# Kernel optimization log

Hardware: AMD Instinct MI355X
Metric: run time of the kernel (lower is better)

## Reference

```python
import jax, jax.numpy as jnp
import numpy as np

STATE_LEN = 128

def _layernorm(x, eps=1e-5):
    m = jnp.mean(x, axis=-1, keepdims=True)
    v = jnp.mean(jnp.square(x - m), axis=-1, keepdims=True)
    return (x - m) * jax.lax.rsqrt(v + eps)

def setup_inputs() -> dict:
    key = jax.random.key(0)
    ks = jax.random.split(key, 20)
    B, S, L = 2, 2048, STATE_LEN
    Din, Dk, Dv, H = 1024, 64, 64, 8
    T = S + 2 * L  # 2304
    x = jax.random.normal(ks[0], (B, T, Din), jnp.float32)
    def w(k, dout):
        return jax.random.normal(k, (H, Din, dout), jnp.float32) / np.sqrt(Din).astype(np.float32)
    inp = {
        'x': x,
        'ln_g':  1.0 + 0.02 * jax.random.normal(ks[1], (H, Din), jnp.float32),
        'ln_b':  0.02 * jax.random.normal(ks[2], (H, Din), jnp.float32),
        'ln_gs': 1.0 + 0.02 * jax.random.normal(ks[3], (H, Din), jnp.float32),
        'ln_bs': 0.02 * jax.random.normal(ks[4], (H, Din), jnp.float32),
        'ln_ge': 1.0 + 0.02 * jax.random.normal(ks[5], (H, Din), jnp.float32),
        'ln_be': 0.02 * jax.random.normal(ks[6], (H, Din), jnp.float32),
        'Wq':   w(ks[7], Dk),  'Wk':   w(ks[8], Dk),  'Wv':   w(ks[9], Dv),
        'Wq_s': w(ks[10], Dk), 'Wk_s': w(ks[11], Dk), 'Wv_s': w(ks[12], Dv),
        'Wq_e': w(ks[13], Dk), 'Wk_e': w(ks[14], Dk), 'Wv_e': w(ks[15], Dv),
        'offset': 0,
    }
    return inp

def _forward(x, ln_g, ln_b, ln_gs, ln_bs, ln_ge, ln_be,
             Wq, Wk, Wv, Wq_s, Wk_s, Wv_s, Wq_e, Wk_e, Wv_e):
    L = STATE_LEN
    B, T, Din = x.shape
    # extract_state: start state, middle sequence, end state
    xs, xm, xe = x[:, :L], x[:, L:T - L], x[:, T - L:]
    # LayerNorm stats are parameter-free; per-head affine applied after
    ns, nm, ne = _layernorm(xs), _layernorm(xm), _layernorm(xe)
    def aff(n, g, b):  # [B,seg,Din] -> [B,H,seg,Din]
        return n[:, None, :, :] * g[None, :, None, :] + b[None, :, None, :]
    hs, hm, he = aff(ns, ln_gs, ln_bs), aff(nm, ln_g, ln_b), aff(ne, ln_ge, ln_be)
    proj = lambda h, W: jnp.einsum('bhsd,hde->bhse', h, W)
    q = jnp.concatenate([proj(hs, Wq_s), proj(hm, Wq), proj(he, Wq_e)], axis=2)
    k = jnp.concatenate([proj(hs, Wk_s), proj(hm, Wk), proj(he, Wk_e)], axis=2)
    v = jnp.concatenate([proj(hs, Wv_s), proj(hm, Wv), proj(he, Wv_e)], axis=2)
    Dk = q.shape[-1]
    scores = jnp.einsum('bhsd,bhtd->bhst', q, k) / jnp.asarray(np.sqrt(Dk), q.dtype)
    # Faithful to the torch code: a FLOAT tril-of-ones mask is passed to SDPA,
    # which ADDS it to the scores (it does not set -inf anywhere).
    mask = jnp.tril(jnp.ones((T, T), scores.dtype))
    att = jax.nn.softmax(scores + mask, axis=-1)
    out = jnp.einsum('bhst,bhtd->bhsd', att, v)  # [B,H,T,Dv]
    H, Dv = out.shape[1], out.shape[3]
    # torch.concat over heads on last dim
    return out.transpose(0, 2, 1, 3).reshape(B, T, H * Dv)

def reference(x, ln_g, ln_b, ln_gs, ln_bs, ln_ge, ln_be,
              Wq, Wk, Wv, Wq_s, Wk_s, Wv_s, Wq_e, Wk_e, Wv_e, offset):
    # offset unused: position_embedders are None in this configuration
    return _forward(x, ln_g, ln_b, ln_gs, ln_bs, ln_ge, ln_be,
                    Wq, Wk, Wv, Wq_s, Wk_s, Wv_s, Wq_e, Wk_e, Wv_e)
```

## Files before the change

### kernel.cpp

```cpp
#include <hip/hip_runtime.h>

#define TSEQ 2304
#define DIN  1024
#define NH   8
#define DD   64
#define NC   1536
#define MROWS 4608
#define L2E  1.44269504f
#define EF   2.71828183f

typedef __attribute__((ext_vector_type(8))) short bf16x8;
typedef __attribute__((ext_vector_type(4))) float f32x4;
typedef __attribute__((ext_vector_type(4))) unsigned short u16x4;

__device__ __forceinline__ unsigned short f2bf(float f){
    union { float f; unsigned int u; } x; x.f = f;
    unsigned int r = x.u + 0x7FFFu + ((x.u >> 16) & 1u);
    return (unsigned short)(r >> 16);
}

__device__ __forceinline__ float exp2raw(float x){
    float r;
    asm("v_exp_f32 %0, %1" : "=v"(r) : "v"(x));
    return r;
}

__device__ __forceinline__ unsigned int cvtpk(float a, float b){
    unsigned int r;
    asm("v_cvt_pk_bf16_f32 %0, %1, %2" : "=v"(r) : "v"(a), "v"(b));
    return r;
}

__device__ __forceinline__ void gload_lds16(const void* g, void* l){
    __builtin_amdgcn_global_load_lds(
        (const __attribute__((address_space(1))) void*)g,
        (__attribute__((address_space(3))) void*)l, 16, 0, 0);
}

struct WArgs {
    const float* W[9];
    const float* g[3];
    const float* bv[3];
};

__global__ __launch_bounds__(256) void k_pre(WArgs a, const float* __restrict__ x,
                                             unsigned short* __restrict__ wb,
                                             float* __restrict__ bias,
                                             unsigned short* __restrict__ nrm)
{
    __shared__ float lds[64][65];
    __shared__ float red[4][64];
    __shared__ float r1[4], r2[4];
    const int bid = blockIdx.x;
    const int tid = threadIdx.x;
    if (bid < 1152){
        const int dt = bid & 15, h = (bid >> 4) & 7, sp = bid >> 7;
        const int seg = sp / 3, proj = sp % 3;
        const float* W = a.W[seg*3 + proj];
        const float* g = a.g[seg];
        const int d0 = dt * 64;
        {
            const int e = tid & 63, rq = tid >> 6;
#pragma unroll
            for (int rr = 0; rr < 16; ++rr){
                const int dl = rr*4 + rq;
                lds[dl][e] = W[((size_t)h*DIN + d0 + dl)*DD + e];
            }
        }
        __syncthreads();
        {
            const int dl = tid & 63, eq = tid >> 6;
            const int n0 = proj*512 + h*64;
            const float gv = g[h*DIN + d0 + dl];
#pragma unroll
            for (int rr = 0; rr < 16; ++rr){
                const int el = eq*16 + rr;
                wb[((size_t)seg*NC + n0 + el)*DIN + d0 + dl] = f2bf(lds[dl][el] * gv);
            }
        }
    } else if (bid < 1224){
        const int u = bid - 1152;
        const int h = u & 7, sp = u >> 3;
        const int seg = sp / 3, proj = sp % 3;
        const float* W  = a.W[seg*3 + proj];
        const float* bv = a.bv[seg];
        const int e = tid & 63, dc = tid >> 6;
        float sum = 0.f;
        for (int i = 0; i < 256; ++i){
            const int d = dc*256 + i;
            sum += bv[h*DIN + d] * W[((size_t)h*DIN + d)*DD + e];
        }
        red[dc][e] = sum;
        __syncthreads();
        if (dc == 0)
            bias[seg*NC + proj*512 + h*64 + e] = red[0][e] + red[1][e] + red[2][e] + red[3][e];
    } else {
        const int row = bid - 1224;
        const float* xr = x + (size_t)row * DIN;
        f32x4 v = *(const f32x4*)&xr[tid*4];
        float s1 = v[0]+v[1]+v[2]+v[3];
        float s2 = v[0]*v[0]+v[1]*v[1]+v[2]*v[2]+v[3]*v[3];
#pragma unroll
        for (int m = 1; m < 64; m <<= 1){ s1 += __shfl_xor(s1, m); s2 += __shfl_xor(s2, m); }
        const int wid = tid >> 6;
        if ((tid & 63) == 0){ r1[wid] = s1; r2[wid] = s2; }
        __syncthreads();
        s1 = r1[0]+r1[1]+r1[2]+r1[3];
        s2 = r2[0]+r2[1]+r2[2]+r2[3];
        const float mean = s1 * (1.f/1024.f);
        const float var  = s2 * (1.f/1024.f) - mean*mean;
        const float rstd = rsqrtf(var + 1e-5f);
        u16x4 ov;
#pragma unroll
        for (int j = 0; j < 4; ++j) ov[j] = f2bf((v[j]-mean)*rstd);
        *(u16x4*)&nrm[(size_t)row*DIN + tid*4] = ov;
    }
}

__global__ __launch_bounds__(256) void k_gemm(
    const unsigned short* __restrict__ A,
    const unsigned short* __restrict__ Wb,
    const float* __restrict__ bias,
    unsigned short* __restrict__ qo,
    unsigned short* __restrict__ ko,
    unsigned short* __restrict__ vt)
{
    __shared__ unsigned short As[128*64];
    __shared__ unsigned short Bs[128*64];
    const int mt = blockIdx.x, nt = blockIdx.y;
    const int row0 = mt*128, n0 = nt*128;
    const int rloc = row0 % TSEQ;
    const int seg = (rloc < 128) ? 0 : (rloc < 2176 ? 1 : 2);
    const unsigned short* Bp = Wb + (size_t)seg * NC * DIN;
    const int tid = threadIdx.x;
    const int wid = tid >> 6, lane = tid & 63;
    const int wr = wid >> 1, wc = wid & 1;
    const int lr = lane & 15, lg = lane >> 4;
    const int rsub = lane >> 3;
    const int cgx  = (lane & 7) ^ rsub;
    f32x4 acc[4][4];
#pragma unroll
    for (int m = 0; m < 4; ++m)
#pragma unroll
        for (int n = 0; n < 4; ++n) acc[m][n] = (f32x4){0.f,0.f,0.f,0.f};

    for (int kt = 0; kt < DIN/64; ++kt){
        const int k0 = kt*64;
        __syncthreads();
#pragma unroll
        for (int i = 0; i < 4; ++i){
            const int c = wid*4 + i;
            const int r = c*8 + rsub;
            gload_lds16(&A [(size_t)(row0 + r)*DIN + k0 + cgx*8], &As[c*512]);
            gload_lds16(&Bp[(size_t)(n0  + r)*DIN + k0 + cgx*8], &Bs[c*512]);
        }
        __syncthreads();
#pragma unroll
        for (int ks = 0; ks < 2; ++ks){
            bf16x8 af[4], bfr[4];
#pragma unroll
            for (int m = 0; m < 4; ++m)
                af[m]  = *(const bf16x8*)&As[(wr*64 + m*16 + lr)*64 + (((ks*4 + lg) ^ (lr & 7))*8)];
#pragma unroll
            for (int n = 0; n < 4; ++n)
                bfr[n] = *(const bf16x8*)&Bs[(wc*64 + n*16 + lr)*64 + (((ks*4 + lg) ^ (lr & 7))*8)];
#pragma unroll
            for (int m = 0; m < 4; ++m)
#pragma unroll
                for (int n = 0; n < 4; ++n)
                    acc[m][n] = __builtin_amdgcn_mfma_f32_16x16x32_bf16(af[m], bfr[n], acc[m][n], 0, 0, 0);
        }
    }
    const int b_ = row0 / TSEQ;
    const int t0 = row0 - b_ * TSEQ;
#pragma unroll
    for (int m = 0; m < 4; ++m){
#pragma unroll
        for (int n = 0; n < 4; ++n){
            const int nglob = n0 + wc*64 + n*16 + lr;
            const float bs = bias[seg*NC + nglob];
            const int proj = nglob >> 9, hh = (nglob >> 6) & 7, e = nglob & 63;
            if (proj < 2){
                unsigned short* op = (proj == 0) ? qo : ko;
                const float scale = (proj == 0) ? 0.125f * L2E : 1.0f;
                const size_t ob = ((size_t)(b_*NH + hh) * TSEQ) * DD + e;
#pragma unroll
                for (int j = 0; j < 4; ++j){
                    const int t = t0 + wr*64 + m*16 + 4*lg + j;
                    op[ob + (size_t)t * DD] = f2bf((acc[m][n][j] + bs) * scale);
                }
            } else {
                unsigned short* vp = vt + ((size_t)(b_*NH + hh)*DD + e)*TSEQ;
                const int t = t0 + wr*64 + m*16 + 4*lg;
                u16x4 pk;
#pragma unroll
                for (int j = 0; j < 4; ++j) pk[j] = f2bf(acc[m][n][j] + bs);
                *(u16x4*)&vp[t] = pk;
            }
        }
    }
}

__global__ __launch_bounds__(256) void k_attn(
    const unsigned short* __restrict__ Q,
    const unsigned short* __restrict__ K,
    const unsigned short* __restrict__ Vt,
    float* __restrict__ po0,
    float* __restrict__ po1,
    float* __restrict__ out2,
    float* __restrict__ pl)
{
    __shared__ unsigned short Ks[2][64*64];
    __shared__ unsigned short Vs[2][64*64];
    __shared__ unsigned short Plds[4][32][72];
    const int qtb = blockIdx.x;
    const int bh  = blockIdx.y;
    const int z   = blockIdx.z;
    const int kt0 = z*12, kt1 = kt0 + 12;
    const int tid  = threadIdx.x;
    const int w    = tid >> 6;
    const int lane = tid & 63;
    const int lr = lane & 15, lg = lane >> 4;
    const size_t qkb = (size_t)bh * TSEQ * DD;
    const size_t vtb = (size_t)bh * DD * TSEQ;
    const int q0w = qtb*128 + w*32;
    const int kd  = qtb*2 + (w >> 1);

    const int rsub = lane >> 3;
    const int cgx  = (lane & 7) ^ rsub;
    const char* Kbase  = (const char*)(K  + qkb);
    const char* Vtbase = (const char*)(Vt + vtb);

    bf16x8 aq[2][2];
#pragma unroll
    for (int qg = 0; qg < 2; ++qg)
#pragma unroll
        for (int ks = 0; ks < 2; ++ks)
            aq[qg][ks] = *(const bf16x8*)&Q[qkb + (size_t)(q0w + qg*16 + lr)*DD + ks*32 + lg*8];

    float lsum[2] = {0.f, 0.f};
    f32x4 o[2][4];
#pragma unroll
    for (int qg = 0; qg < 2; ++qg)
#pragma unroll
        for (int nd = 0; nd < 4; ++nd) o[qg][nd] = (f32x4){0.f,0.f,0.f,0.f};

    auto stage = [&](int kt, int b){
        const int kn = kt*64;
#pragma unroll
        for (int i = 0; i < 2; ++i){
            const int c = w*2 + i;
            const int r = c*8 + rsub;
            gload_lds16(Kbase  + (size_t)(kn + r)*128 + cgx*16,              &Ks[b][c*512]);
            gload_lds16(Vtbase + (size_t)r*(TSEQ*2) + (size_t)kn*2 + cgx*16, &Vs[b][c*512]);
        }
    };

    stage(kt0, 0);
    __syncthreads();

    unsigned int* PldsW = (unsigned int*)&Plds[w][0][0];

    int buf = 0;
    for (int kt = kt0; kt < kt1; ++kt){
        const int kc0 = kt*64;
        if (kt + 1 < kt1) stage(kt + 1, buf ^ 1);
        bf16x8 bk[2][4];
#pragma unroll
        for (int ks = 0; ks < 2; ++ks)
#pragma unroll
            for (int ns = 0; ns < 4; ++ns)
                bk[ks][ns] = *(const bf16x8*)&Ks[buf][(ns*16 + lr)*64 + (((4*ks + lg) ^ (lr & 7))*8)];
        f32x4 s[2][4];
#pragma unroll
        for (int qg = 0; qg < 2; ++qg)
#pragma unroll
            for (int ns = 0; ns < 4; ++ns) s[qg][ns] = (f32x4){0.f,0.f,0.f,0.f};
#pragma unroll
        for (int qg = 0; qg < 2; ++qg)
#pragma unroll
            for (int ks = 0; ks < 2; ++ks)
#pragma unroll
                for (int ns = 0; ns < 4; ++ns)
                    s[qg][ns] = __builtin_amdgcn_mfma_f32_16x16x32_bf16(bk[ks][ns], aq[qg][ks], s[qg][ns], 0, 0, 0);
        if (kt == kd){
#pragma unroll
            for (int qg = 0; qg < 2; ++qg){
                lsum[qg] *= EF;
#pragma unroll
                for (int nd = 0; nd < 4; ++nd)
#pragma unroll
                    for (int j = 0; j < 4; ++j) o[qg][nd][j] *= EF;
                const int qr = q0w + qg*16 + lr;
#pragma unroll
                for (int ns = 0; ns < 4; ++ns){
                    const int kb = kc0 + ns*16 + 4*lg;
                    float p0 = exp2raw(s[qg][ns][0] + ((kb + 0 <= qr) ? L2E : 0.f));
                    float p1 = exp2raw(s[qg][ns][1] + ((kb + 1 <= qr) ? L2E : 0.f));
                    float p2 = exp2raw(s[qg][ns][2] + ((kb + 2 <= qr) ? L2E : 0.f));
                    float p3 = exp2raw(s[qg][ns][3] + ((kb + 3 <= qr) ? L2E : 0.f));
                    lsum[qg] += (p0 + p1) + (p2 + p3);
                    PldsW[(qg*16 + lr)*36 + ns*8 + 2*lg + 0] = cvtpk(p0, p1);
                    PldsW[(qg*16 + lr)*36 + ns*8 + 2*lg + 1] = cvtpk(p2, p3);
                }
            }
        } else {
#pragma unroll
            for (int qg = 0; qg < 2; ++qg){
#pragma unroll
                for (int ns = 0; ns < 4; ++ns){
                    float p0 = exp2raw(s[qg][ns][0]);
                    float p1 = exp2raw(s[qg][ns][1]);
                    float p2 = exp2raw(s[qg][ns][2]);
                    float p3 = exp2raw(s[qg][ns][3]);
                    lsum[qg] += (p0 + p1) + (p2 + p3);
                    PldsW[(qg*16 + lr)*36 + ns*8 + 2*lg + 0] = cvtpk(p0, p1);
                    PldsW[(qg*16 + lr)*36 + ns*8 + 2*lg + 1] = cvtpk(p2, p3);
                }
            }
        }
        bf16x8 bv[2][4];
#pragma unroll
        for (int ks = 0; ks < 2; ++ks)
#pragma unroll
            for (int nd = 0; nd < 4; ++nd)
                bv[ks][nd] = *(const bf16x8*)&Vs[buf][(nd*16 + lr)*64 + (((4*ks + lg) ^ (lr & 7))*8)];
#pragma unroll
        for (int qg = 0; qg < 2; ++qg){
            bf16x8 pa0 = *(const bf16x8*)&Plds[w][qg*16 + lr][0*32 + lg*8];
            bf16x8 pa1 = *(const bf16x8*)&Plds[w][qg*16 + lr][1*32 + lg*8];
#pragma unroll
            for (int nd = 0; nd < 4; ++nd){
                o[qg][nd] = __builtin_amdgcn_mfma_f32_16x16x32_bf16(pa0, bv[0][nd], o[qg][nd], 0, 0, 0);
                o[qg][nd] = __builtin_amdgcn_mfma_f32_16x16x32_bf16(pa1, bv[1][nd], o[qg][nd], 0, 0, 0);
            }
        }
        __syncthreads();
        buf ^= 1;
    }
    if (kd >= kt1){
#pragma unroll
        for (int qg = 0; qg < 2; ++qg){
            lsum[qg] *= EF;
#pragma unroll
            for (int nd = 0; nd < 4; ++nd)
#pragma unroll
                for (int j = 0; j < 4; ++j) o[qg][nd][j] *= EF;
        }
    }
#pragma unroll
    for (int qg = 0; qg < 2; ++qg){
        lsum[qg] += __shfl_xor(lsum[qg], 16);
        lsum[qg] += __shfl_xor(lsum[qg], 32);
    }
    const int pbase = ((z*16 + bh)*18 + qtb)*128 + w*32;
    if (lg == 0){
        pl[pbase + 0*16 + lr] = lsum[0];
        pl[pbase + 1*16 + lr] = lsum[1];
    }
    if (z < 2){
        float* po = (z == 0) ? po0 : po1;
        const size_t tb = ((size_t)(bh*18 + qtb)*128 + w*32) * 64;
#pragma unroll
        for (int qg = 0; qg < 2; ++qg)
#pragma unroll
            for (int j = 0; j < 4; ++j)
#pragma unroll
                for (int nd = 0; nd < 4; ++nd)
                    po[tb + (size_t)(qg*16 + 4*lg + j)*64 + nd*16 + lr] = o[qg][nd][j];
    } else {
        const int b_ = bh >> 3, hh = bh & 7;
#pragma unroll
        for (int qg = 0; qg < 2; ++qg){
#pragma unroll
            for (int j = 0; j < 4; ++j){
                const int t = q0w + qg*16 + 4*lg + j;
                const size_t ob = ((size_t)(b_*TSEQ + t))*512 + hh*64;
#pragma unroll
                for (int nd = 0; nd < 4; ++nd)
                    out2[ob + nd*16 + lr] = o[qg][nd][j];
            }
        }
    }
}

__global__ __launch_bounds__(256) void k_comb(
    const float* __restrict__ po0, const float* __restrict__ po1,
    const float* __restrict__ pl, float* __restrict__ out)
{
    const int qt = blockIdx.x, bh = blockIdx.y;
    const int b_ = bh >> 3, hh = bh & 7;
    const int tid = threadIdx.x;
    const int row = tid >> 2;
    const int c0  = (tid & 3) * 16;
    const int t128  = qt >> 1;
    const int rowin = (qt & 1)*64 + row;
    const int plb = (bh*18 + t128)*128 + rowin;
    const float inv = 1.0f / (pl[plb] + pl[(16*18*128) + plb] + pl[(2*16*18*128) + plb]);
    const size_t tb = ((size_t)(bh*18 + t128)*128 + rowin)*64 + c0;
    const size_t ob = ((size_t)(b_*TSEQ + qt*64 + row))*512 + hh*64 + c0;
#pragma unroll
    for (int i = 0; i < 4; ++i){
        f32x4 a = *(const f32x4*)&po0[tb + i*4];
        f32x4 b = *(const f32x4*)&po1[tb + i*4];
        f32x4 c = *(const f32x4*)&out[ob + i*4];
        f32x4 r;
#pragma unroll
        for (int j = 0; j < 4; ++j) r[j] = (a[j] + b[j] + c[j]) * inv;
        *(f32x4*)&out[ob + i*4] = r;
    }
}

extern "C" void kernel_launch(void* const* d_in, const int* in_sizes, int n_in,
                              void* d_out, int out_size, void* d_ws, size_t ws_size,
                              hipStream_t stream)
{
    const float* x     = (const float*)d_in[0];
    const float* ln_g  = (const float*)d_in[1];
    const float* ln_b  = (const float*)d_in[2];
    const float* ln_gs = (const float*)d_in[3];
    const float* ln_bs = (const float*)d_in[4];
    const float* ln_ge = (const float*)d_in[5];
    const float* ln_be = (const float*)d_in[6];
    const float* Wq    = (const float*)d_in[7];
    const float* Wk    = (const float*)d_in[8];
    const float* Wv    = (const float*)d_in[9];
    const float* Wq_s  = (const float*)d_in[10];
    const float* Wk_s  = (const float*)d_in[11];
    const float* Wv_s  = (const float*)d_in[12];
    const float* Wq_e  = (const float*)d_in[13];
    const float* Wk_e  = (const float*)d_in[14];
    const float* Wv_e  = (const float*)d_in[15];

    uint8_t* w = (uint8_t*)d_ws;
    unsigned short* nrm = (unsigned short*)(w);
    unsigned short* wb  = (unsigned short*)(w + 9437184);
    float*          bia = (float*)        (w + 18874368);
    unsigned short* q_  = (unsigned short*)(w + 18892800);
    unsigned short* k_  = (unsigned short*)(w + 23611392);
    unsigned short* vt_ = (unsigned short*)(w + 28329984);
    float*          pl  = (float*)        (w + 33048576);
    float*          po0 = (float*)        (w);
    float*          po1 = (float*)        (w + 9437184);

    WArgs wa;
    wa.W[0] = Wq_s; wa.W[1] = Wk_s; wa.W[2] = Wv_s;
    wa.W[3] = Wq;   wa.W[4] = Wk;   wa.W[5] = Wv;
    wa.W[6] = Wq_e; wa.W[7] = Wk_e; wa.W[8] = Wv_e;
    wa.g[0] = ln_gs; wa.g[1] = ln_g; wa.g[2] = ln_ge;
    wa.bv[0] = ln_bs; wa.bv[1] = ln_b; wa.bv[2] = ln_be;

    float* out = (float*)d_out;
    k_pre <<<dim3(5832),      dim3(256), 0, stream>>>(wa, x, wb, bia, nrm);
    k_gemm<<<dim3(36, 12),    dim3(256), 0, stream>>>(nrm, wb, bia, q_, k_, vt_);
    k_attn<<<dim3(18, 16, 3), dim3(256), 0, stream>>>(q_, k_, vt_, po0, po1, out, pl);
    k_comb<<<dim3(36, 16),    dim3(256), 0, stream>>>(po0, po1, pl, out);
}
```

Baseline: 99.57 us.

## Switch attention to 32x32x16 MFMA and keep P in registers via permlane32 swap

```diff
diff --git a/kernel.cpp b/kernel.cpp
--- a/kernel.cpp
+++ b/kernel.cpp
@@ -11,7 +11,9 @@
 
 typedef __attribute__((ext_vector_type(8))) short bf16x8;
 typedef __attribute__((ext_vector_type(4))) float f32x4;
+typedef __attribute__((ext_vector_type(16))) float f32x16;
 typedef __attribute__((ext_vector_type(4))) unsigned short u16x4;
+typedef __attribute__((ext_vector_type(4))) unsigned int u32x4;
 
 __device__ __forceinline__ unsigned short f2bf(float f){
     union { float f; unsigned int u; } x; x.f = f;
@@ -212,7 +214,6 @@
 {
     __shared__ unsigned short Ks[2][64*64];
     __shared__ unsigned short Vs[2][64*64];
-    __shared__ unsigned short Plds[4][32][72];
     const int qtb = blockIdx.x;
     const int bh  = blockIdx.y;
     const int z   = blockIdx.z;
@@ -220,7 +221,8 @@
     const int tid  = threadIdx.x;
     const int w    = tid >> 6;
     const int lane = tid & 63;
-    const int lr = lane & 15, lg = lane >> 4;
+    const int l31  = lane & 31;
+    const int h    = lane >> 5;
     const size_t qkb = (size_t)bh * TSEQ * DD;
     const size_t vtb = (size_t)bh * DD * TSEQ;
     const int q0w = qtb*128 + w*32;
@@ -231,19 +233,15 @@
     const char* Kbase  = (const char*)(K  + qkb);
     const char* Vtbase = (const char*)(Vt + vtb);
 
-    bf16x8 aq[2][2];
-#pragma unroll
-    for (int qg = 0; qg < 2; ++qg)
-#pragma unroll
-        for (int ks = 0; ks < 2; ++ks)
-            aq[qg][ks] = *(const bf16x8*)&Q[qkb + (size_t)(q0w + qg*16 + lr)*DD + ks*32 + lg*8];
-
-    float lsum[2] = {0.f, 0.f};
-    f32x4 o[2][4];
-#pragma unroll
-    for (int qg = 0; qg < 2; ++qg)
-#pragma unroll
-        for (int nd = 0; nd < 4; ++nd) o[qg][nd] = (f32x4){0.f,0.f,0.f,0.f};
+    bf16x8 aq[4];
+#pragma unroll
+    for (int ds = 0; ds < 4; ++ds)
+        aq[ds] = *(const bf16x8*)&Q[qkb + (size_t)(q0w + l31)*DD + ds*16 + h*8];
+
+    float lsum = 0.f;
+    f32x16 o0, o1;
+#pragma unroll
+    for (int r = 0; r < 16; ++r){ o0[r] = 0.f; o1[r] = 0.f; }
 
     auto stage = [&](int kt, int b){
         const int kn = kt*64;
@@ -259,127 +257,94 @@
     stage(kt0, 0);
     __syncthreads();
 
-    unsigned int* PldsW = (unsigned int*)&Plds[w][0][0];
+    const int rowA = l31 * 64;
 
     int buf = 0;
     for (int kt = kt0; kt < kt1; ++kt){
         const int kc0 = kt*64;
         if (kt + 1 < kt1) stage(kt + 1, buf ^ 1);
-        bf16x8 bk[2][4];
-#pragma unroll
-        for (int ks = 0; ks < 2; ++ks)
-#pragma unroll
-            for (int ns = 0; ns < 4; ++ns)
-                bk[ks][ns] = *(const bf16x8*)&Ks[buf][(ns*16 + lr)*64 + (((4*ks + lg) ^ (lr & 7))*8)];
-        f32x4 s[2][4];
-#pragma unroll
-        for (int qg = 0; qg < 2; ++qg)
-#pragma unroll
-            for (int ns = 0; ns < 4; ++ns) s[qg][ns] = (f32x4){0.f,0.f,0.f,0.f};
-#pragma unroll
-        for (int qg = 0; qg < 2; ++qg)
-#pragma unroll
-            for (int ks = 0; ks < 2; ++ks)
-#pragma unroll
-                for (int ns = 0; ns < 4; ++ns)
-                    s[qg][ns] = __builtin_amdgcn_mfma_f32_16x16x32_bf16(bk[ks][ns], aq[qg][ks], s[qg][ns], 0, 0, 0);
+        f32x16 s0, s1;
+#pragma unroll
+        for (int r = 0; r < 16; ++r){ s0[r] = 0.f; s1[r] = 0.f; }
+#pragma unroll
+        for (int ds = 0; ds < 4; ++ds){
+            const int sx = (((ds*2 + h) ^ (lane & 7)) * 8);
+            bf16x8 kf0 = *(const bf16x8*)&Ks[buf][rowA + sx];
+            bf16x8 kf1 = *(const bf16x8*)&Ks[buf][rowA + 2048 + sx];
+            s0 = __builtin_amdgcn_mfma_f32_32x32x16_bf16(kf0, aq[ds], s0, 0, 0, 0);
+            s1 = __builtin_amdgcn_mfma_f32_32x32x16_bf16(kf1, aq[ds], s1, 0, 0, 0);
+        }
         if (kt == kd){
-#pragma unroll
-            for (int qg = 0; qg < 2; ++qg){
-                lsum[qg] *= EF;
-#pragma unroll
-                for (int nd = 0; nd < 4; ++nd)
-#pragma unroll
-                    for (int j = 0; j < 4; ++j) o[qg][nd][j] *= EF;
-                const int qr = q0w + qg*16 + lr;
-#pragma unroll
-                for (int ns = 0; ns < 4; ++ns){
-                    const int kb = kc0 + ns*16 + 4*lg;
-                    float p0 = exp2raw(s[qg][ns][0] + ((kb + 0 <= qr) ? L2E : 0.f));
-                    float p1 = exp2raw(s[qg][ns][1] + ((kb + 1 <= qr) ? L2E : 0.f));
-                    float p2 = exp2raw(s[qg][ns][2] + ((kb + 2 <= qr) ? L2E : 0.f));
-                    float p3 = exp2raw(s[qg][ns][3] + ((kb + 3 <= qr) ? L2E : 0.f));
-                    lsum[qg] += (p0 + p1) + (p2 + p3);
-                    PldsW[(qg*16 + lr)*36 + ns*8 + 2*lg + 0] = cvtpk(p0, p1);
-                    PldsW[(qg*16 + lr)*36 + ns*8 + 2*lg + 1] = cvtpk(p2, p3);
-                }
+            lsum *= EF;
+#pragma unroll
+            for (int r = 0; r < 16; ++r){ o0[r] *= EF; o1[r] *= EF; }
+            const int qr = q0w + l31;
+#pragma unroll
+            for (int r = 0; r < 16; ++r){
+                const int kk = kc0 + (r&3) + 8*(r>>2) + 4*h;
+                const float p0 = exp2raw(s0[r] + ((kk      <= qr) ? L2E : 0.f));
+                const float p1 = exp2raw(s1[r] + ((kk + 32 <= qr) ? L2E : 0.f));
+                s0[r] = p0; s1[r] = p1;
+                lsum += p0 + p1;
             }
         } else {
 #pragma unroll
-            for (int qg = 0; qg < 2; ++qg){
-#pragma unroll
-                for (int ns = 0; ns < 4; ++ns){
-                    float p0 = exp2raw(s[qg][ns][0]);
-                    float p1 = exp2raw(s[qg][ns][1]);
-                    float p2 = exp2raw(s[qg][ns][2]);
-                    float p3 = exp2raw(s[qg][ns][3]);
-                    lsum[qg] += (p0 + p1) + (p2 + p3);
-                    PldsW[(qg*16 + lr)*36 + ns*8 + 2*lg + 0] = cvtpk(p0, p1);
-                    PldsW[(qg*16 + lr)*36 + ns*8 + 2*lg + 1] = cvtpk(p2, p3);
-                }
-            }
-        }
-        bf16x8 bv[2][4];
-#pragma unroll
-        for (int ks = 0; ks < 2; ++ks)
-#pragma unroll
-            for (int nd = 0; nd < 4; ++nd)
-                bv[ks][nd] = *(const bf16x8*)&Vs[buf][(nd*16 + lr)*64 + (((4*ks + lg) ^ (lr & 7))*8)];
-#pragma unroll
-        for (int qg = 0; qg < 2; ++qg){
-            bf16x8 pa0 = *(const bf16x8*)&Plds[w][qg*16 + lr][0*32 + lg*8];
-            bf16x8 pa1 = *(const bf16x8*)&Plds[w][qg*16 + lr][1*32 + lg*8];
-#pragma unroll
-            for (int nd = 0; nd < 4; ++nd){
-                o[qg][nd] = __builtin_amdgcn_mfma_f32_16x16x32_bf16(pa0, bv[0][nd], o[qg][nd], 0, 0, 0);
-                o[qg][nd] = __builtin_amdgcn_mfma_f32_16x16x32_bf16(pa1, bv[1][nd], o[qg][nd], 0, 0, 0);
-            }
+            for (int r = 0; r < 16; ++r){
+                const float p0 = exp2raw(s0[r]);
+                const float p1 = exp2raw(s1[r]);
+                s0[r] = p0; s1[r] = p1;
+                lsum += p0 + p1;
+            }
+        }
+#pragma unroll
+        for (int ks = 0; ks < 4; ++ks){
+            const int rb = (ks & 1) * 8;
+            unsigned int a01, a23, b01, b23;
+            if (ks < 2){
+                a01 = cvtpk(s0[rb+0], s0[rb+1]); a23 = cvtpk(s0[rb+2], s0[rb+3]);
+                b01 = cvtpk(s0[rb+4], s0[rb+5]); b23 = cvtpk(s0[rb+6], s0[rb+7]);
+            } else {
+                a01 = cvtpk(s1[rb+0], s1[rb+1]); a23 = cvtpk(s1[rb+2], s1[rb+3]);
+                b01 = cvtpk(s1[rb+4], s1[rb+5]); b23 = cvtpk(s1[rb+6], s1[rb+7]);
+            }
+            asm("v_permlane32_swap_b32 %0, %1" : "+v"(a01), "+v"(b01));
+            asm("v_permlane32_swap_b32 %0, %1" : "+v"(a23), "+v"(b23));
+            u32x4 fw; fw[0] = a01; fw[1] = a23; fw[2] = b01; fw[3] = b23;
+            bf16x8 pa = __builtin_bit_cast(bf16x8, fw);
+            const int sx = (((ks*2 + h) ^ (lane & 7)) * 8);
+            bf16x8 vf0 = *(const bf16x8*)&Vs[buf][rowA + sx];
+            bf16x8 vf1 = *(const bf16x8*)&Vs[buf][rowA + 2048 + sx];
+            o0 = __builtin_amdgcn_mfma_f32_32x32x16_bf16(pa, vf0, o0, 0, 0, 0);
+            o1 = __builtin_amdgcn_mfma_f32_32x32x16_bf16(pa, vf1, o1, 0, 0, 0);
         }
         __syncthreads();
         buf ^= 1;
     }
     if (kd >= kt1){
-#pragma unroll
-        for (int qg = 0; qg < 2; ++qg){
-            lsum[qg] *= EF;
-#pragma unroll
-            for (int nd = 0; nd < 4; ++nd)
-#pragma unroll
-                for (int j = 0; j < 4; ++j) o[qg][nd][j] *= EF;
-        }
-    }
-#pragma unroll
-    for (int qg = 0; qg < 2; ++qg){
-        lsum[qg] += __shfl_xor(lsum[qg], 16);
-        lsum[qg] += __shfl_xor(lsum[qg], 32);
-    }
+        lsum *= EF;
+#pragma unroll
+        for (int r = 0; r < 16; ++r){ o0[r] *= EF; o1[r] *= EF; }
+    }
+    lsum += __shfl_xor(lsum, 32);
     const int pbase = ((z*16 + bh)*18 + qtb)*128 + w*32;
-    if (lg == 0){
-        pl[pbase + 0*16 + lr] = lsum[0];
-        pl[pbase + 1*16 + lr] = lsum[1];
-    }
+    if (h == 0) pl[pbase + l31] = lsum;
     if (z < 2){
         float* po = (z == 0) ? po0 : po1;
         const size_t tb = ((size_t)(bh*18 + qtb)*128 + w*32) * 64;
 #pragma unroll
-        for (int qg = 0; qg < 2; ++qg)
-#pragma unroll
-            for (int j = 0; j < 4; ++j)
-#pragma unroll
-                for (int nd = 0; nd < 4; ++nd)
-                    po[tb + (size_t)(qg*16 + 4*lg + j)*64 + nd*16 + lr] = o[qg][nd][j];
+        for (int r = 0; r < 16; ++r){
+            const int qloc = (r&3) + 8*(r>>2) + 4*h;
+            po[tb + (size_t)qloc*64 + l31]      = o0[r];
+            po[tb + (size_t)qloc*64 + 32 + l31] = o1[r];
+        }
     } else {
         const int b_ = bh >> 3, hh = bh & 7;
 #pragma unroll
-        for (int qg = 0; qg < 2; ++qg){
-#pragma unroll
-            for (int j = 0; j < 4; ++j){
-                const int t = q0w + qg*16 + 4*lg + j;
-                const size_t ob = ((size_t)(b_*TSEQ + t))*512 + hh*64;
-#pragma unroll
-                for (int nd = 0; nd < 4; ++nd)
-                    out2[ob + nd*16 + lr] = o[qg][nd][j];
-            }
+        for (int r = 0; r < 16; ++r){
+            const int qloc = (r&3) + 8*(r>>2) + 4*h;
+            const size_t ob = ((size_t)(b_*TSEQ + q0w + qloc))*512 + hh*64;
+            out2[ob + l31]      = o0[r];
+            out2[ob + 32 + l31] = o1[r];
         }
     }
 }
```

New measurement: 97.61 us, median of 2. -2.0%, faster.
